# Optimization experiments

Hardware: AMD Instinct MI355X
Metric: run time of the kernel (lower is better)

## Reference

```python
import jax, jax.numpy as jnp
import numpy as np
import math

D_MODEL = 2048
N_HEADS = 16
HEAD_DIM = D_MODEL // N_HEADS  # 128
SEQ_LEN = 4096
BATCH = 4


def rotate_half(x):
    x1, x2 = x[..., : x.shape[-1] // 2], x[..., x.shape[-1] // 2 :]
    return jnp.concatenate((-x2, x1), axis=-1)


def rope_cos_sin(seq_len, head_dim, dtype=jnp.float32):
    inv_freq = 1.0 / (10000.0 ** (jnp.arange(0, head_dim, 2, dtype=jnp.float32) / head_dim))
    freqs = jnp.arange(seq_len, dtype=jnp.float32)[:, None] * inv_freq[None, :]  # [S, D/2]
    emb = jnp.concatenate((freqs, freqs), axis=-1)  # [S, D]
    return jnp.cos(emb).astype(dtype), jnp.sin(emb).astype(dtype)


def setup_inputs() -> dict:
    key = jax.random.key(0)
    kx, kq, kk, kv = jax.random.split(key, 4)
    x = jax.random.normal(kx, (BATCH, SEQ_LEN, D_MODEL), dtype=jnp.float32)
    s = 1.0 / math.sqrt(D_MODEL)
    # torch Linear weight: [out_features, in_features]
    w_q = jax.random.uniform(kq, (HEAD_DIM, D_MODEL), minval=-s, maxval=s, dtype=jnp.float32)
    w_k = jax.random.uniform(kk, (HEAD_DIM, D_MODEL), minval=-s, maxval=s, dtype=jnp.float32)
    w_v = jax.random.uniform(kv, (HEAD_DIM, D_MODEL), minval=-s, maxval=s, dtype=jnp.float32)
    return {"x": x, "w_q": w_q, "w_k": w_k, "w_v": w_v}


def reference(x, w_q, w_k, w_v):
    B, S, _ = x.shape
    scale = 1.0 / math.sqrt(HEAD_DIM)
    # projections: x @ W^T  -> [B, S, head_dim]
    q = jnp.einsum('bsd,hd->bsh', x, w_q)
    k = jnp.einsum('bsd,hd->bsh', x, w_k)
    v = jnp.einsum('bsd,hd->bsh', x, w_v)
    cos, sin = rope_cos_sin(S, HEAD_DIM, x.dtype)  # [S, head_dim]
    q = q * cos + rotate_half(q) * sin
    k = k * cos + rotate_half(k) * sin
    scores = jnp.einsum('bqh,bkh->bqk', q, k) * scale  # [B, S, S]
    causal = jnp.tril(jnp.ones((S, S), dtype=bool))
    scores = jnp.where(causal[None, :, :], scores, -jnp.inf)
    attn = jax.nn.softmax(scores, axis=-1)
    out = jnp.einsum('bqk,bkh->bqh', attn, v)  # [B, S, head_dim]
    return out
```

## Files before the change

kernel.cpp:

```cpp
#include <hip/hip_runtime.h>
#include <hip/hip_bf16.h>

#define BATCH 4
#define SEQ 4096
#define DMODEL 2048
#define HD 128
#define BS (BATCH*SEQ)

typedef __attribute__((ext_vector_type(8))) short short8;
typedef __attribute__((ext_vector_type(4))) float f32x4;
typedef __attribute__((ext_vector_type(4))) float float4v;
typedef unsigned short u16;
typedef unsigned int u32;

#define LOG2E 1.4426950408889634f
#define SCALE 0.08838834764831845f

__device__ __forceinline__ u16 f2bf(float f){
  u32 u = __builtin_bit_cast(u32, f);
  u32 r = (u + 0x7FFFu + ((u >> 16) & 1u)) >> 16;
  return (u16)r;
}

__device__ __forceinline__ void gload16(const void* gptr, void* lptr){
  __builtin_amdgcn_global_load_lds((const __attribute__((address_space(1))) void*)gptr,
                                   (__attribute__((address_space(3))) void*)lptr, 16, 0, 0);
}

__global__ __launch_bounds__(256) void k_tab(float2* __restrict__ tab){
  int i = blockIdx.x*256 + threadIdx.x;
  int s = i >> 6, j = i & 63;
  float invf = (float)pow(10000.0, -(double)j/64.0);
  float ang  = (float)s * invf;
  double a = (double)ang;
  tab[i] = make_float2((float)cos(a), (float)sin(a));
}

__global__ __launch_bounds__(256) void k_cvtx(const float* __restrict__ x, u16* __restrict__ xb){
  size_t i = (size_t)blockIdx.x*256 + threadIdx.x;
  const float4v* xp = (const float4v*)x;
  float4v a = xp[i*2], c = xp[i*2+1];
  short8 o;
  o[0]=(short)f2bf(a[0]); o[1]=(short)f2bf(a[1]); o[2]=(short)f2bf(a[2]); o[3]=(short)f2bf(a[3]);
  o[4]=(short)f2bf(c[0]); o[5]=(short)f2bf(c[1]); o[6]=(short)f2bf(c[2]); o[7]=(short)f2bf(c[3]);
  *(short8*)(xb + i*8) = o;
}

__global__ __launch_bounds__(256) void k_cvtw(const float* __restrict__ wq, const float* __restrict__ wk,
                                              const float* __restrict__ wv, u16* __restrict__ wb){
  int i = blockIdx.x*256 + threadIdx.x;
  int m = i >> 18; int r = i & 262143;
  const float* s = (m==0) ? wq : ((m==1) ? wk : wv);
  wb[i] = f2bf(s[r]);
}

__global__ __launch_bounds__(256) void k_gemm(
    const u16* __restrict__ xb, const u16* __restrict__ wb, const float2* __restrict__ tab,
    u16* __restrict__ qb, u16* __restrict__ kb, u16* __restrict__ vt)
{
  __shared__ u16 lA[128*64];
  __shared__ u16 lW[128*64];
  const int tid = threadIdx.x;
  const int wsel = blockIdx.y;
  const size_t M0 = (size_t)blockIdx.x * 128;
  const u16* Wm = wb + (size_t)wsel * (HD*DMODEL);
  const int w = tid >> 6, lane = tid & 63, lr = lane & 15, lg = lane >> 4;

  f32x4 acc[2][8];
  #pragma unroll
  for (int i=0;i<2;i++)
    #pragma unroll
    for (int j=0;j<8;j++) acc[i][j] = f32x4{0.f,0.f,0.f,0.f};

  const int Lb = tid*16;
  int srow[4], soff[4];
  #pragma unroll
  for (int i=0;i<4;i++){
    int L = i*4096 + Lb;
    int row = L >> 7, cb = L & 127;
    int scb = cb ^ ((row & 7) << 4);
    srow[i] = row; soff[i] = scb >> 1;
  }

  for (int k0 = 0; k0 < DMODEL; k0 += 64){
    #pragma unroll
    for (int i=0;i<4;i++){
      gload16(xb + (M0 + srow[i])*DMODEL + k0 + soff[i], ((char*)lA) + i*4096 + Lb);
      gload16(Wm + (size_t)srow[i]*DMODEL + k0 + soff[i], ((char*)lW) + i*4096 + Lb);
    }
    __syncthreads();
    short8 afr[2][2], bfr[8][2];
    #pragma unroll
    for (int rf=0; rf<2; rf++)
      #pragma unroll
      for (int ks=0; ks<2; ks++){
        int r = w*32 + rf*16 + lr;
        int byte = r*128 + ((ks*64 + lg*16) ^ ((r&7)<<4));
        afr[rf][ks] = *(const short8*)((const char*)lA + byte);
      }
    #pragma unroll
    for (int nf=0; nf<8; nf++)
      #pragma unroll
      for (int ks=0; ks<2; ks++){
        int r = nf*16 + lr;
        int byte = r*128 + ((ks*64 + lg*16) ^ ((r&7)<<4));
        bfr[nf][ks] = *(const short8*)((const char*)lW + byte);
      }
    #pragma unroll
    for (int rf=0; rf<2; rf++)
      #pragma unroll
      for (int nf=0; nf<8; nf++){
        acc[rf][nf] = __builtin_amdgcn_mfma_f32_16x16x32_bf16(afr[rf][0], bfr[nf][0], acc[rf][nf], 0,0,0);
        acc[rf][nf] = __builtin_amdgcn_mfma_f32_16x16x32_bf16(afr[rf][1], bfr[nf][1], acc[rf][nf], 0,0,0);
      }
    __syncthreads();
  }

  if (wsel < 2){
    u16* dst = (wsel == 0) ? qb : kb;
    #pragma unroll
    for (int rf=0; rf<2; rf++){
      #pragma unroll
      for (int reg=0; reg<4; reg++){
        size_t grow = M0 + w*32 + rf*16 + lg*4 + reg;
        int spos = (int)(grow & (SEQ-1));
        #pragma unroll
        for (int cf=0; cf<4; cf++){
          int j = cf*16 + lr;
          float2 cs = tab[spos*64 + j];
          float lo = acc[rf][cf][reg];
          float hi = acc[rf][cf+4][reg];
          dst[grow*HD + j]      = f2bf(lo*cs.x - hi*cs.y);
          dst[grow*HD + j + 64] = f2bf(hi*cs.x + lo*cs.y);
        }
      }
    }
  } else {
    #pragma unroll
    for (int rf=0; rf<2; rf++)
      #pragma unroll
      for (int reg=0; reg<4; reg++){
        size_t grow = M0 + w*32 + rf*16 + lg*4 + reg;
        size_t b = grow >> 12;
        size_t spos = grow & (SEQ-1);
        #pragma unroll
        for (int cf=0; cf<8; cf++){
          int col = cf*16 + lr;
          vt[(b*HD + col)*SEQ + spos] = f2bf(acc[rf][cf][reg]);
        }
      }
  }
}

__global__ __launch_bounds__(256) void k_attn(
    const u16* __restrict__ qbuf, const u16* __restrict__ kb, const u16* __restrict__ vt,
    float* __restrict__ Opart, float2* __restrict__ ml)
{
  __shared__ u16 lK[64*128];
  __shared__ u16 lV[128*64];
  __shared__ u16 lP[4][16*64];
  const int tid = threadIdx.x;
  const int bid = blockIdx.x;
  const int x = bid & 7, idx = bid >> 3;
  const int b = x >> 1, half = x & 1;
  const int qt = 63 - (idx >> 1);
  const int sp = (idx & 1) + 2*half;
  const int qbn = b*64 + qt;
  const int w = tid >> 6, lane = tid & 63, lr = lane & 15, lg = lane >> 4;

  const int n = qt + 1, cbase = n >> 2, crem = n & 3;
  const int cnt = cbase + (sp < crem ? 1 : 0);
  const int klo = sp*cbase + (sp < crem ? sp : crem);
  const int khi = klo + cnt;
  const size_t prow0 = ((size_t)qbn*4 + sp)*64;

  if (cnt == 0){
    if (lr == 0){
      #pragma unroll
      for (int reg=0; reg<4; reg++)
        ml[prow0 + w*16 + lg*4 + reg] = make_float2(-1e30f, 0.f);
    }
    return;
  }

  const size_t qrow = (size_t)b*SEQ + qt*64 + w*16 + lr;
  short8 aq[4];
  #pragma unroll
  for (int ks=0; ks<4; ks++)
    aq[ks] = *(const short8*)(qbuf + qrow*HD + ks*32 + lg*8);

  f32x4 accO[8];
  #pragma unroll
  for (int i=0;i<8;i++) accO[i] = f32x4{0.f,0.f,0.f,0.f};
  float m2[4]   = {-1e30f,-1e30f,-1e30f,-1e30f};
  float lsum[4] = {0.f,0.f,0.f,0.f};

  const int Lb = tid*16;
  const float cfac = SCALE * LOG2E;

  for (int kt = klo; kt < khi; kt++){
    #pragma unroll
    for (int i=0;i<4;i++){
      int L = i*4096 + Lb;
      { int row = L >> 8, cb = L & 255;
        int scb = cb ^ ((row & 7) << 4);
        gload16(kb + ((size_t)b*SEQ + kt*64 + row)*HD + (scb>>1), ((char*)lK) + L); }
      { int row = L >> 7, cb = L & 127;
        int scb = cb ^ ((row & 7) << 4);
        gload16(vt + ((size_t)b*HD + row)*SEQ + kt*64 + (scb>>1), ((char*)lV) + L); }
    }
    __syncthreads();

    f32x4 sc[4];
    #pragma unroll
    for (int nf=0; nf<4; nf++){
      sc[nf] = f32x4{0.f,0.f,0.f,0.f};
      #pragma unroll
      for (int ks=0; ks<4; ks++){
        int r = nf*16 + lr;
        int byte = r*256 + ((ks*64 + lg*16) ^ ((r&7)<<4));
        short8 bk = *(const short8*)((const char*)lK + byte);
        sc[nf] = __builtin_amdgcn_mfma_f32_16x16x32_bf16(aq[ks], bk, sc[nf], 0,0,0);
      }
      sc[nf] *= cfac;
    }
    if (kt == qt){
      #pragma unroll
      for (int nf=0; nf<4; nf++)
        #pragma unroll
        for (int reg=0; reg<4; reg++){
          int col = nf*16 + lr;
          int row = w*16 + lg*4 + reg;
          if (col > row) sc[nf][reg] = -1e30f;
        }
    }
    float al[4];
    #pragma unroll
    for (int reg=0; reg<4; reg++){
      float v = fmaxf(fmaxf(sc[0][reg], sc[1][reg]), fmaxf(sc[2][reg], sc[3][reg]));
      v = fmaxf(v, __shfl_xor(v, 1));
      v = fmaxf(v, __shfl_xor(v, 2));
      v = fmaxf(v, __shfl_xor(v, 4));
      v = fmaxf(v, __shfl_xor(v, 8));
      float mnew = fmaxf(m2[reg], v);
      al[reg] = exp2f(m2[reg] - mnew);
      m2[reg] = mnew;
    }
    float prs[4] = {0.f,0.f,0.f,0.f};
    #pragma unroll
    for (int nf=0; nf<4; nf++)
      #pragma unroll
      for (int reg=0; reg<4; reg++){
        float p = exp2f(sc[nf][reg] - m2[reg]);
        prs[reg] += p;
        int r = lg*4 + reg;
        int byte = r*128 + ((nf*32 + lr*2) ^ ((r&7)<<4));
        *(u16*)(((char*)lP[w]) + byte) = f2bf(p);
      }
    f32x4 alv = f32x4{al[0], al[1], al[2], al[3]};
    #pragma unroll
    for (int reg=0; reg<4; reg++){
      float v = prs[reg];
      v += __shfl_xor(v, 1);
      v += __shfl_xor(v, 2);
      v += __shfl_xor(v, 4);
      v += __shfl_xor(v, 8);
      lsum[reg] = lsum[reg]*al[reg] + v;
    }
    #pragma unroll
    for (int cf=0; cf<8; cf++) accO[cf] *= alv;

    short8 pa[2];
    #pragma unroll
    for (int ks=0; ks<2; ks++){
      int byte = lr*128 + ((ks*64 + lg*16) ^ ((lr&7)<<4));
      pa[ks] = *(const short8*)(((const char*)lP[w]) + byte);
    }
    #pragma unroll
    for (int cf=0; cf<8; cf++){
      #pragma unroll
      for (int ks=0; ks<2; ks++){
        int d = cf*16 + lr;
        int byte = d*128 + ((ks*64 + lg*16) ^ ((d&7)<<4));
        short8 bv = *(const short8*)(((const char*)lV) + byte);
        accO[cf] = __builtin_amdgcn_mfma_f32_16x16x32_bf16(pa[ks], bv, accO[cf], 0,0,0);
      }
    }
    __syncthreads();
  }

  #pragma unroll
  for (int reg=0; reg<4; reg++){
    size_t pr = prow0 + w*16 + lg*4 + reg;
    #pragma unroll
    for (int cf=0; cf<8; cf++)
      Opart[pr*HD + cf*16 + lr] = accO[cf][reg];
  }
  if (lr == 0){
    #pragma unroll
    for (int reg=0; reg<4; reg++)
      ml[prow0 + w*16 + lg*4 + reg] = make_float2(m2[reg], lsum[reg]);
  }
}

__global__ __launch_bounds__(256) void k_comb(
    const float* __restrict__ Opart, const float2* __restrict__ ml, float* __restrict__ out)
{
  const int t = threadIdx.x;
  const int r = blockIdx.x*8 + (t >> 5);
  const int c = (t & 31)*4;
  const int qbn = r >> 6, rr = r & 63;
  float m[4], l[4], M = -1e30f;
  #pragma unroll
  for (int s=0; s<4; s++){
    float2 v = ml[((size_t)qbn*4 + s)*64 + rr];
    m[s] = v.x; l[s] = v.y;
    M = fmaxf(M, m[s]);
  }
  float L = 0.f;
  #pragma unroll
  for (int s=0; s<4; s++){ m[s] = exp2f(m[s] - M); L += l[s]*m[s]; }
  const float inv = 1.0f / L;
  f32x4 acc = f32x4{0.f,0.f,0.f,0.f};
  #pragma unroll
  for (int s=0; s<4; s++){
    f32x4 o = *(const f32x4*)(Opart + (((size_t)qbn*4 + s)*64 + rr)*(size_t)HD + c);
    float sc = m[s]*inv;
    acc += o * sc;
  }
  *(f32x4*)(out + (size_t)r*HD + c) = acc;
}

extern "C" void kernel_launch(void* const* d_in, const int* in_sizes, int n_in,
                              void* d_out, int out_size, void* d_ws, size_t ws_size,
                              hipStream_t stream){
  const float* x  = (const float*)d_in[0];
  const float* wq = (const float*)d_in[1];
  const float* wk = (const float*)d_in[2];
  const float* wv = (const float*)d_in[3];
  float* out = (float*)d_out;
  char* ws = (char*)d_ws;

  size_t off = 0;
  u16* xb = (u16*)(ws + off); off += (size_t)BS*DMODEL*2;
  u16* wb = (u16*)(ws + off); off += (size_t)3*HD*DMODEL*2;
  float2* tab = (float2*)(ws + off); off += (size_t)SEQ*64*8;
  u16* qb = (u16*)(ws + off); off += (size_t)BS*HD*2;
  u16* kb = (u16*)(ws + off); off += (size_t)BS*HD*2;
  u16* vt = (u16*)(ws + off); off += (size_t)BS*HD*2;
  float* Opart = (float*)(ws + off); off += (size_t)1024*64*HD*4;
  float2* ml   = (float2*)(ws + off); off += (size_t)1024*64*8;
  if (ws_size < off) return;

  hipLaunchKernelGGL(k_tab,  dim3(1024),  dim3(256), 0, stream, tab);
  hipLaunchKernelGGL(k_cvtx, dim3(16384), dim3(256), 0, stream, x, xb);
  hipLaunchKernelGGL(k_cvtw, dim3(3072),  dim3(256), 0, stream, wq, wk, wv, wb);
  hipLaunchKernelGGL(k_gemm, dim3(128,3), dim3(256), 0, stream, xb, wb, tab, qb, kb, vt);
  hipLaunchKernelGGL(k_attn, dim3(1024),  dim3(256), 0, stream, qb, kb, vt, Opart, ml);
  hipLaunchKernelGGL(k_comb, dim3(2048),  dim3(256), 0, stream, Opart, ml, out);
}
```

Baseline: 138.4 us.

## Fuse fp32-to-bf16 x conversion into QKV GEMM with double-buffered LDS

Drops the separate kernel that converts x to bf16. The GEMM now loads fp32 x directly into LDS and converts it to bf16 in registers. Each block computes all three Q/K/V projections for 64 rows instead of one projection for 128 rows, so x is read once rather than three times. A double-buffered 128KB LDS pipeline overlaps loads with MFMA work, at the cost of larger LDS use (lower occupancy) and doubled x load bytes per tile.

```diff
diff --git a/kernel.cpp b/kernel.cpp
--- a/kernel.cpp
+++ b/kernel.cpp
@@ -36,16 +36,6 @@
   tab[i] = make_float2((float)cos(a), (float)sin(a));
 }
 
-__global__ __launch_bounds__(256) void k_cvtx(const float* __restrict__ x, u16* __restrict__ xb){
-  size_t i = (size_t)blockIdx.x*256 + threadIdx.x;
-  const float4v* xp = (const float4v*)x;
-  float4v a = xp[i*2], c = xp[i*2+1];
-  short8 o;
-  o[0]=(short)f2bf(a[0]); o[1]=(short)f2bf(a[1]); o[2]=(short)f2bf(a[2]); o[3]=(short)f2bf(a[3]);
-  o[4]=(short)f2bf(c[0]); o[5]=(short)f2bf(c[1]); o[6]=(short)f2bf(c[2]); o[7]=(short)f2bf(c[3]);
-  *(short8*)(xb + i*8) = o;
-}
-
 __global__ __launch_bounds__(256) void k_cvtw(const float* __restrict__ wq, const float* __restrict__ wk,
                                               const float* __restrict__ wv, u16* __restrict__ wb){
   int i = blockIdx.x*256 + threadIdx.x;
@@ -55,101 +45,119 @@
 }
 
 __global__ __launch_bounds__(256) void k_gemm(
-    const u16* __restrict__ xb, const u16* __restrict__ wb, const float2* __restrict__ tab,
+    const float* __restrict__ x, const u16* __restrict__ wb, const float2* __restrict__ tab,
     u16* __restrict__ qb, u16* __restrict__ kb, u16* __restrict__ vt)
 {
-  __shared__ u16 lA[128*64];
-  __shared__ u16 lW[128*64];
+  __shared__ char lds[2][65536];
   const int tid = threadIdx.x;
-  const int wsel = blockIdx.y;
-  const size_t M0 = (size_t)blockIdx.x * 128;
-  const u16* Wm = wb + (size_t)wsel * (HD*DMODEL);
+  const size_t M0 = (size_t)blockIdx.x * 64;
   const int w = tid >> 6, lane = tid & 63, lr = lane & 15, lg = lane >> 4;
-
-  f32x4 acc[2][8];
-  #pragma unroll
-  for (int i=0;i<2;i++)
-    #pragma unroll
-    for (int j=0;j<8;j++) acc[i][j] = f32x4{0.f,0.f,0.f,0.f};
-
-  const int Lb = tid*16;
-  int srow[4], soff[4];
+  const int h = w & 1, g = w >> 1;
+
+  int nfs[6];
+  nfs[0] = g*8 + 2*h;     nfs[1] = nfs[0] + 4;
+  nfs[2] = g*8 + 2*h + 1; nfs[3] = nfs[2] + 4;
+  nfs[4] = 16 + 2*w;      nfs[5] = nfs[4] + 1;
+
+  int aoff[4], adst[4], woff[12], wdst[12];
   #pragma unroll
   for (int i=0;i<4;i++){
-    int L = i*4096 + Lb;
+    int L = i*4096 + tid*16;
+    int row = L >> 8, cb = L & 255;
+    int scb = cb ^ ((row & 7) << 5);
+    aoff[i] = (int)((M0 + row)*DMODEL) + (scb >> 2);
+    adst[i] = L;
+  }
+  #pragma unroll
+  for (int i=0;i<12;i++){
+    int L = i*4096 + tid*16;
     int row = L >> 7, cb = L & 127;
     int scb = cb ^ ((row & 7) << 4);
-    srow[i] = row; soff[i] = scb >> 1;
-  }
-
-  for (int k0 = 0; k0 < DMODEL; k0 += 64){
-    #pragma unroll
-    for (int i=0;i<4;i++){
-      gload16(xb + (M0 + srow[i])*DMODEL + k0 + soff[i], ((char*)lA) + i*4096 + Lb);
-      gload16(Wm + (size_t)srow[i]*DMODEL + k0 + soff[i], ((char*)lW) + i*4096 + Lb);
+    woff[i] = row*DMODEL + (scb >> 1);
+    wdst[i] = 16384 + L;
+  }
+
+  f32x4 acc[4][6];
+  #pragma unroll
+  for (int i=0;i<4;i++)
+    #pragma unroll
+    for (int j=0;j<6;j++) acc[i][j] = f32x4{0.f,0.f,0.f,0.f};
+
+  {
+    char* base = lds[0];
+    #pragma unroll
+    for (int i=0;i<4;i++)  gload16(x + aoff[i], base + adst[i]);
+    #pragma unroll
+    for (int i=0;i<12;i++) gload16(wb + woff[i], base + wdst[i]);
+  }
+  __syncthreads();
+
+  int cur = 0;
+  for (int t=0; t<32; t++){
+    if (t < 31){
+      char* base = lds[cur^1];
+      const int k0 = (t+1)*64;
+      #pragma unroll
+      for (int i=0;i<4;i++)  gload16(x + aoff[i] + k0, base + adst[i]);
+      #pragma unroll
+      for (int i=0;i<12;i++) gload16(wb + woff[i] + k0, base + wdst[i]);
+    }
+    const char* lA = lds[cur];
+    const char* lW = lds[cur] + 16384;
+
+    short8 af[2][4];
+    #pragma unroll
+    for (int ks=0;ks<2;ks++)
+      #pragma unroll
+      for (int rf=0;rf<4;rf++){
+        int r = rf*16 + lr;
+        int byte = r*256 + ((ks*128 + lg*32) ^ ((r&7)<<5));
+        f32x4 va = *(const f32x4*)(lA + byte);
+        f32x4 vb = *(const f32x4*)(lA + byte + 16);
+        short8 tt;
+        tt[0]=(short)f2bf(va[0]); tt[1]=(short)f2bf(va[1]); tt[2]=(short)f2bf(va[2]); tt[3]=(short)f2bf(va[3]);
+        tt[4]=(short)f2bf(vb[0]); tt[5]=(short)f2bf(vb[1]); tt[6]=(short)f2bf(vb[2]); tt[7]=(short)f2bf(vb[3]);
+        af[ks][rf] = tt;
+      }
+    #pragma unroll
+    for (int j=0;j<6;j++){
+      int rw = nfs[j]*16 + lr;
+      #pragma unroll
+      for (int ks=0;ks<2;ks++){
+        int byte = rw*128 + ((ks*64 + lg*16) ^ ((lr&7)<<4));
+        short8 bf = *(const short8*)(lW + byte);
+        #pragma unroll
+        for (int rf=0;rf<4;rf++)
+          acc[rf][j] = __builtin_amdgcn_mfma_f32_16x16x32_bf16(af[ks][rf], bf, acc[rf][j], 0,0,0);
+      }
     }
     __syncthreads();
-    short8 afr[2][2], bfr[8][2];
-    #pragma unroll
-    for (int rf=0; rf<2; rf++)
-      #pragma unroll
-      for (int ks=0; ks<2; ks++){
-        int r = w*32 + rf*16 + lr;
-        int byte = r*128 + ((ks*64 + lg*16) ^ ((r&7)<<4));
-        afr[rf][ks] = *(const short8*)((const char*)lA + byte);
-      }
-    #pragma unroll
-    for (int nf=0; nf<8; nf++)
-      #pragma unroll
-      for (int ks=0; ks<2; ks++){
-        int r = nf*16 + lr;
-        int byte = r*128 + ((ks*64 + lg*16) ^ ((r&7)<<4));
-        bfr[nf][ks] = *(const short8*)((const char*)lW + byte);
-      }
-    #pragma unroll
-    for (int rf=0; rf<2; rf++)
-      #pragma unroll
-      for (int nf=0; nf<8; nf++){
-        acc[rf][nf] = __builtin_amdgcn_mfma_f32_16x16x32_bf16(afr[rf][0], bfr[nf][0], acc[rf][nf], 0,0,0);
-        acc[rf][nf] = __builtin_amdgcn_mfma_f32_16x16x32_bf16(afr[rf][1], bfr[nf][1], acc[rf][nf], 0,0,0);
-      }
-    __syncthreads();
-  }
-
-  if (wsel < 2){
-    u16* dst = (wsel == 0) ? qb : kb;
-    #pragma unroll
-    for (int rf=0; rf<2; rf++){
-      #pragma unroll
-      for (int reg=0; reg<4; reg++){
-        size_t grow = M0 + w*32 + rf*16 + lg*4 + reg;
-        int spos = (int)(grow & (SEQ-1));
-        #pragma unroll
-        for (int cf=0; cf<4; cf++){
-          int j = cf*16 + lr;
-          float2 cs = tab[spos*64 + j];
-          float lo = acc[rf][cf][reg];
-          float hi = acc[rf][cf+4][reg];
-          dst[grow*HD + j]      = f2bf(lo*cs.x - hi*cs.y);
-          dst[grow*HD + j + 64] = f2bf(hi*cs.x + lo*cs.y);
-        }
-      }
-    }
-  } else {
-    #pragma unroll
-    for (int rf=0; rf<2; rf++)
-      #pragma unroll
-      for (int reg=0; reg<4; reg++){
-        size_t grow = M0 + w*32 + rf*16 + lg*4 + reg;
-        size_t b = grow >> 12;
-        size_t spos = grow & (SEQ-1);
-        #pragma unroll
-        for (int cf=0; cf<8; cf++){
-          int col = cf*16 + lr;
-          vt[(b*HD + col)*SEQ + spos] = f2bf(acc[rf][cf][reg]);
-        }
-      }
-  }
+    cur ^= 1;
+  }
+
+  u16* dst = (g == 0) ? qb : kb;
+  #pragma unroll
+  for (int rf=0; rf<4; rf++)
+    #pragma unroll
+    for (int reg=0; reg<4; reg++){
+      size_t grow = M0 + rf*16 + lg*4 + reg;
+      int spos = (int)(grow & (SEQ-1));
+      size_t b = grow >> 12;
+      #pragma unroll
+      for (int p=0; p<2; p++){
+        int j = (2*h + p)*16 + lr;
+        float2 cs = tab[spos*64 + j];
+        float lo = acc[rf][2*p][reg];
+        float hi = acc[rf][2*p+1][reg];
+        dst[grow*HD + j]      = f2bf(lo*cs.x - hi*cs.y);
+        dst[grow*HD + j + 64] = f2bf(hi*cs.x + lo*cs.y);
+      }
+      #pragma unroll
+      for (int jj=0; jj<2; jj++){
+        int col = (2*w + jj)*16 + lr;
+        vt[(b*HD + col)*SEQ + spos] = f2bf(acc[rf][4+jj][reg]);
+      }
+    }
 }
 
 __global__ __launch_bounds__(256) void k_attn(
@@ -342,7 +350,6 @@
   char* ws = (char*)d_ws;
 
   size_t off = 0;
-  u16* xb = (u16*)(ws + off); off += (size_t)BS*DMODEL*2;
   u16* wb = (u16*)(ws + off); off += (size_t)3*HD*DMODEL*2;
   float2* tab = (float2*)(ws + off); off += (size_t)SEQ*64*8;
   u16* qb = (u16*)(ws + off); off += (size_t)BS*HD*2;
@@ -353,9 +360,8 @@
   if (ws_size < off) return;
 
   hipLaunchKernelGGL(k_tab,  dim3(1024),  dim3(256), 0, stream, tab);
-  hipLaunchKernelGGL(k_cvtx, dim3(16384), dim3(256), 0, stream, x, xb);
   hipLaunchKernelGGL(k_cvtw, dim3(3072),  dim3(256), 0, stream, wq, wk, wv, wb);
-  hipLaunchKernelGGL(k_gemm, dim3(128,3), dim3(256), 0, stream, xb, wb, tab, qb, kb, vt);
+  hipLaunchKernelGGL(k_gemm, dim3(256),   dim3(256), 0, stream, x, wb, tab, qb, kb, vt);
   hipLaunchKernelGGL(k_attn, dim3(1024),  dim3(256), 0, stream, qb, kb, vt, Opart, ml);
   hipLaunchKernelGGL(k_comb, dim3(2048),  dim3(256), 0, stream, Opart, ml, out);
 }
```

Result: faster. 130.1 us (-6.0%).

## Fuse fp32-to-bf16 conversion of x into the projection GEMM

Applied to the files above, without the earlier changes.

Removes the separate x conversion kernel and its bf16 workspace buffer. The GEMM now loads fp32 x straight from global memory, converts it in registers and writes it swizzled into LDS. The 1D grid is remapped so that the three weight matrices sharing an M tile go to the same XCD, which should let them reuse x in L2. The trade-off is that each fp32 x tile is read three times (once per weight matrix), and the register-staged loads are no longer asynchronous LDS loads, which may expose latency.

```diff
diff --git a/kernel.cpp b/kernel.cpp
--- a/kernel.cpp
+++ b/kernel.cpp
@@ -8,6 +8,7 @@
 #define BS (BATCH*SEQ)
 
 typedef __attribute__((ext_vector_type(8))) short short8;
+typedef __attribute__((ext_vector_type(4))) short short4v;
 typedef __attribute__((ext_vector_type(4))) float f32x4;
 typedef __attribute__((ext_vector_type(4))) float float4v;
 typedef unsigned short u16;
@@ -36,16 +37,6 @@
   tab[i] = make_float2((float)cos(a), (float)sin(a));
 }
 
-__global__ __launch_bounds__(256) void k_cvtx(const float* __restrict__ x, u16* __restrict__ xb){
-  size_t i = (size_t)blockIdx.x*256 + threadIdx.x;
-  const float4v* xp = (const float4v*)x;
-  float4v a = xp[i*2], c = xp[i*2+1];
-  short8 o;
-  o[0]=(short)f2bf(a[0]); o[1]=(short)f2bf(a[1]); o[2]=(short)f2bf(a[2]); o[3]=(short)f2bf(a[3]);
-  o[4]=(short)f2bf(c[0]); o[5]=(short)f2bf(c[1]); o[6]=(short)f2bf(c[2]); o[7]=(short)f2bf(c[3]);
-  *(short8*)(xb + i*8) = o;
-}
-
 __global__ __launch_bounds__(256) void k_cvtw(const float* __restrict__ wq, const float* __restrict__ wk,
                                               const float* __restrict__ wv, u16* __restrict__ wb){
   int i = blockIdx.x*256 + threadIdx.x;
@@ -54,39 +45,58 @@
   wb[i] = f2bf(s[r]);
 }
 
-__global__ __launch_bounds__(256) void k_gemm(
-    const u16* __restrict__ xb, const u16* __restrict__ wb, const float2* __restrict__ tab,
+__global__ __launch_bounds__(256,2) void k_gemm(
+    const float* __restrict__ x, const u16* __restrict__ wb, const float2* __restrict__ tab,
     u16* __restrict__ qb, u16* __restrict__ kb, u16* __restrict__ vt)
 {
-  __shared__ u16 lA[128*64];
-  __shared__ u16 lW[128*64];
+  __shared__ char lds[32768];
   const int tid = threadIdx.x;
-  const int wsel = blockIdx.y;
-  const size_t M0 = (size_t)blockIdx.x * 128;
-  const u16* Wm = wb + (size_t)wsel * (HD*DMODEL);
+  const int bid = blockIdx.x;
+  const int xcd = bid & 7, idx = bid >> 3;
+  const int mloc = idx / 3, ng = idx - mloc*3;
+  const int mg = xcd*16 + mloc;
+  const size_t M0 = (size_t)mg * 128;
+  const u16* Wm = wb + (size_t)ng * (HD*DMODEL);
   const int w = tid >> 6, lane = tid & 63, lr = lane & 15, lg = lane >> 4;
 
-  f32x4 acc[2][8];
-  #pragma unroll
-  for (int i=0;i<2;i++)
-    #pragma unroll
-    for (int j=0;j<8;j++) acc[i][j] = f32x4{0.f,0.f,0.f,0.f};
-
-  const int Lb = tid*16;
-  int srow[4], soff[4];
+  const float* aptr[8];
+  int awb[8];
+  #pragma unroll
+  for (int i=0;i<8;i++){
+    int L = i*4096 + tid*16;
+    int row = L >> 8, col = (L & 255) >> 2;
+    aptr[i] = x + (M0 + row)*DMODEL + col;
+    awb[i]  = row*128 + ((col*2) ^ ((row & 7) << 4));
+  }
+  int woff[4], wdst[4];
   #pragma unroll
   for (int i=0;i<4;i++){
-    int L = i*4096 + Lb;
+    int L = i*4096 + tid*16;
     int row = L >> 7, cb = L & 127;
     int scb = cb ^ ((row & 7) << 4);
-    srow[i] = row; soff[i] = scb >> 1;
-  }
-
-  for (int k0 = 0; k0 < DMODEL; k0 += 64){
-    #pragma unroll
-    for (int i=0;i<4;i++){
-      gload16(xb + (M0 + srow[i])*DMODEL + k0 + soff[i], ((char*)lA) + i*4096 + Lb);
-      gload16(Wm + (size_t)srow[i]*DMODEL + k0 + soff[i], ((char*)lW) + i*4096 + Lb);
+    woff[i] = row*DMODEL + (scb >> 1);
+    wdst[i] = 16384 + L;
+  }
+
+  f32x4 acc[2][8];
+  #pragma unroll
+  for (int i=0;i<2;i++)
+    #pragma unroll
+    for (int j=0;j<8;j++) acc[i][j] = f32x4{0.f,0.f,0.f,0.f};
+
+  for (int t=0; t<32; t++){
+    const int k0 = t*64;
+    float4v av[8];
+    #pragma unroll
+    for (int i=0;i<8;i++) av[i] = *(const float4v*)(aptr[i] + k0);
+    #pragma unroll
+    for (int i=0;i<4;i++) gload16(Wm + woff[i] + k0, lds + wdst[i]);
+    #pragma unroll
+    for (int i=0;i<8;i++){
+      short4v o;
+      o[0]=(short)f2bf(av[i][0]); o[1]=(short)f2bf(av[i][1]);
+      o[2]=(short)f2bf(av[i][2]); o[3]=(short)f2bf(av[i][3]);
+      *(short4v*)(lds + awb[i]) = o;
     }
     __syncthreads();
     short8 afr[2][2], bfr[8][2];
@@ -95,16 +105,14 @@
       #pragma unroll
       for (int ks=0; ks<2; ks++){
         int r = w*32 + rf*16 + lr;
-        int byte = r*128 + ((ks*64 + lg*16) ^ ((r&7)<<4));
-        afr[rf][ks] = *(const short8*)((const char*)lA + byte);
+        afr[rf][ks] = *(const short8*)(lds + r*128 + ((ks*64 + lg*16) ^ ((r&7)<<4)));
       }
     #pragma unroll
     for (int nf=0; nf<8; nf++)
       #pragma unroll
       for (int ks=0; ks<2; ks++){
         int r = nf*16 + lr;
-        int byte = r*128 + ((ks*64 + lg*16) ^ ((r&7)<<4));
-        bfr[nf][ks] = *(const short8*)((const char*)lW + byte);
+        bfr[nf][ks] = *(const short8*)(lds + 16384 + r*128 + ((ks*64 + lg*16) ^ ((r&7)<<4)));
       }
     #pragma unroll
     for (int rf=0; rf<2; rf++)
@@ -116,8 +124,8 @@
     __syncthreads();
   }
 
-  if (wsel < 2){
-    u16* dst = (wsel == 0) ? qb : kb;
+  if (ng < 2){
+    u16* dst = (ng == 0) ? qb : kb;
     #pragma unroll
     for (int rf=0; rf<2; rf++){
       #pragma unroll
@@ -342,7 +350,6 @@
   char* ws = (char*)d_ws;
 
   size_t off = 0;
-  u16* xb = (u16*)(ws + off); off += (size_t)BS*DMODEL*2;
   u16* wb = (u16*)(ws + off); off += (size_t)3*HD*DMODEL*2;
   float2* tab = (float2*)(ws + off); off += (size_t)SEQ*64*8;
   u16* qb = (u16*)(ws + off); off += (size_t)BS*HD*2;
@@ -353,9 +360,8 @@
   if (ws_size < off) return;
 
   hipLaunchKernelGGL(k_tab,  dim3(1024),  dim3(256), 0, stream, tab);
-  hipLaunchKernelGGL(k_cvtx, dim3(16384), dim3(256), 0, stream, x, xb);
   hipLaunchKernelGGL(k_cvtw, dim3(3072),  dim3(256), 0, stream, wq, wk, wv, wb);
-  hipLaunchKernelGGL(k_gemm, dim3(128,3), dim3(256), 0, stream, xb, wb, tab, qb, kb, vt);
+  hipLaunchKernelGGL(k_gemm, dim3(384),   dim3(256), 0, stream, x, wb, tab, qb, kb, vt);
   hipLaunchKernelGGL(k_attn, dim3(1024),  dim3(256), 0, stream, qb, kb, vt, Opart, ml);
   hipLaunchKernelGGL(k_comb, dim3(2048),  dim3(256), 0, stream, Opart, ml, out);
 }
```

Measured after the change: 122.4 us. 11.6% less time.
